# Kernel optimization log

Measured on AMD Instinct MI355X. Metric: run time of the kernel, lower is better.

The kernel has to match this reference:

```python
import jax, jax.numpy as jnp
import numpy as np
from jax import lax

SCORE_TH = 0.05
IOU_TH = 0.5
MAX_DET = 100  # fixed keep budget per class (torch version is variable-length; we pad)
BBOX_STD = jnp.array([0.1, 0.1, 0.2, 0.2], dtype=jnp.float32)


def setup_inputs() -> dict:
    key = jax.random.key(0)
    k1, k2, k3, k4 = jax.random.split(key, 4)
    A, C, H, W = 200000, 80, 768, 768
    # sigmoid-like scores, skewed low so the 0.05 threshold is meaningful
    classification = jax.random.uniform(k1, (A, C), dtype=jnp.float32) ** 4
    regression = jax.random.normal(k2, (A, 4), dtype=jnp.float32)
    ctr = jax.random.uniform(k3, (A, 2), dtype=jnp.float32, minval=0.0, maxval=float(W))
    wh = jax.random.uniform(k4, (A, 2), dtype=jnp.float32, minval=8.0, maxval=128.0)
    anchors = jnp.concatenate([ctr - 0.5 * wh, ctr + 0.5 * wh], axis=-1)  # valid x1y1x2y2
    return {"classification": classification, "regression": regression,
            "anchors": anchors, "img_h": H, "img_w": W}


def _decode_clip(anchors, regression, img_h, img_w):
    # BBoxTransform: RetinaNet delta decode with std [0.1,0.1,0.2,0.2], then ClipBoxes
    wa = anchors[:, 2] - anchors[:, 0]
    ha = anchors[:, 3] - anchors[:, 1]
    cxa = anchors[:, 0] + 0.5 * wa
    cya = anchors[:, 1] + 0.5 * ha
    d = regression * BBOX_STD
    cx = cxa + d[:, 0] * wa
    cy = cya + d[:, 1] * ha
    w = jnp.exp(d[:, 2]) * wa
    h = jnp.exp(d[:, 3]) * ha
    boxes = jnp.stack([cx - 0.5 * w, cy - 0.5 * h, cx + 0.5 * w, cy + 0.5 * h], axis=-1)
    lim = jnp.array([img_w, img_h, img_w, img_h], dtype=boxes.dtype)
    return jnp.clip(boxes, 0.0, lim)


def _nms_one(scores_c, boxes, areas):
    # greedy NMS for one class over all A anchors; fixed MAX_DET iterations
    s0 = jnp.where(scores_c > SCORE_TH, scores_c, -1.0)

    def step(s, _):
        i = jnp.argmax(s)
        valid = s[i] > 0.0
        b = boxes[i]
        xx1 = jnp.maximum(b[0], boxes[:, 0])
        yy1 = jnp.maximum(b[1], boxes[:, 1])
        xx2 = jnp.minimum(b[2], boxes[:, 2])
        yy2 = jnp.minimum(b[3], boxes[:, 3])
        inter = jnp.maximum(xx2 - xx1, 0.0) * jnp.maximum(yy2 - yy1, 0.0)
        iou = inter / (areas[i] + areas - inter)
        supp = (iou > IOU_TH) & valid
        s = jnp.where(supp, -1.0, s).at[i].set(-1.0)
        return s, (i, valid)

    _, (idx, val) = lax.scan(step, s0, None, length=MAX_DET)
    return idx, val  # [MAX_DET] int, [MAX_DET] bool


def _forward(classification, regression, anchors, img_h, img_w):
    boxes = _decode_clip(anchors, regression, img_h, img_w)  # [A,4]
    # NMS index selection is non-differentiable (as in torch); stop_gradient the selection path
    boxes_ng = lax.stop_gradient(boxes)
    scores_ng = lax.stop_gradient(classification)
    areas = (boxes_ng[:, 2] - boxes_ng[:, 0]) * (boxes_ng[:, 3] - boxes_ng[:, 1])
    idx, val = jax.vmap(_nms_one, in_axes=(1, None, None))(scores_ng, boxes_ng, areas)  # [C,M]
    C = classification.shape[1]
    sel_scores = jnp.take_along_axis(classification.T, idx, axis=1) * val          # [C,M]
    sel_boxes = boxes[idx] * val[..., None]                                        # [C,M,4]
    class_ids = jnp.where(val, jnp.arange(C, dtype=jnp.int32)[:, None], -1)        # [C,M]
    # torch returns variable-length concatenations; we return fixed-size padded
    # equivalents (invalid slots: score=0, class=-1, box=0)
    return sel_scores.reshape(-1), class_ids.reshape(-1), sel_boxes.reshape(-1, 4)


def reference(classification, regression, anchors, img_h, img_w):
    return _forward(classification, regression, anchors, img_h, img_w)
```

## Files before the change

kernel.cpp:

```cpp
#include <hip/hip_runtime.h>
#include <float.h>
#include <math.h>

#define SCORE_TH 0.05f
#define IOU_TH   0.5f
#define MAXD     100
#define CAP      512
#define HI_TH    0.996f
#define SWALK    192
#define NWORDS   3
#define CNT_STRIDE 16

__device__ __forceinline__ float4 decode_box(float4 an, float4 r, float W, float H)
{
    float wa = an.z - an.x, ha = an.w - an.y;
    float cxa = an.x + 0.5f * wa, cya = an.y + 0.5f * ha;
    float cx = cxa + r.x * 0.1f * wa;
    float cy = cya + r.y * 0.1f * ha;
    float w  = expf(r.z * 0.2f) * wa;
    float h  = expf(r.w * 0.2f) * ha;
    float x1 = cx - 0.5f * w, y1 = cy - 0.5f * h;
    float x2 = cx + 0.5f * w, y2 = cy + 0.5f * h;
    x1 = fminf(fmaxf(x1, 0.f), W);
    y1 = fminf(fmaxf(y1, 0.f), H);
    x2 = fminf(fmaxf(x2, 0.f), W);
    y2 = fminf(fmaxf(y2, 0.f), H);
    return make_float4(x1, y1, x2, y2);
}

template<int CC>
__global__ __launch_bounds__(256)
void k_compact(const float4* __restrict__ cls4, float2* __restrict__ cand,
               int* __restrict__ cnt, int* __restrict__ loflag,
               int C_rt, int total4)
{
    const int C = CC ? CC : C_rt;
    __shared__ unsigned char lflag[256];
    for (int i = threadIdx.x; i < C; i += blockDim.x) lflag[i] = 0;
    __syncthreads();

    const int gstride = gridDim.x * blockDim.x;
    const int gtid = blockIdx.x * blockDim.x + threadIdx.x;

    for (int j0 = gtid; j0 < total4; j0 += 4 * gstride) {
        int j1 = j0 + gstride, j2 = j0 + 2 * gstride, j3 = j0 + 3 * gstride;
        bool ok1 = j1 < total4, ok2 = j2 < total4, ok3 = j3 < total4;
        float4 v0 = cls4[j0];
        float4 v1 = ok1 ? cls4[j1] : make_float4(0.f, 0.f, 0.f, 0.f);
        float4 v2 = ok2 ? cls4[j2] : make_float4(0.f, 0.f, 0.f, 0.f);
        float4 v3 = ok3 ? cls4[j3] : make_float4(0.f, 0.f, 0.f, 0.f);

        #pragma unroll
        for (int w = 0; w < 4; w++) {
            float4 v = (w == 0) ? v0 : (w == 1) ? v1 : (w == 2) ? v2 : v3;
            if (w == 1 && !ok1) break;
            if (w == 2 && !ok2) break;
            if (w == 3 && !ok3) break;
            unsigned b = (unsigned)(j0 + w * gstride) * 4u;
            int c = (int)(b % (unsigned)C);
            int a = (int)(b / (unsigned)C);
            float s[4] = {v.x, v.y, v.z, v.w};
            #pragma unroll
            for (int j = 0; j < 4; j++) {
                float sc = s[j];
                if (sc > HI_TH) {
                    int pos = atomicAdd(&cnt[c * CNT_STRIDE], 1);
                    if (pos < CAP) cand[(size_t)c * CAP + pos] = make_float2(sc, __int_as_float(a));
                } else if (sc > SCORE_TH) {
                    lflag[c] = 1;
                }
                c++; if (c == C) { c = 0; a++; }
            }
        }
    }
    __syncthreads();
    for (int i = threadIdx.x; i < C; i += blockDim.x)
        if (lflag[i]) loflag[i] = 1;
}

__device__ void fallback_class(const float* __restrict__ cls,
                               const float4* __restrict__ anch, const float4* __restrict__ reg,
                               float W, float H, int A, int C, int c,
                               float* __restrict__ out)
{
    __shared__ float kx1[MAXD], ky1[MAXD], kx2[MAXD], ky2[MAXD], kar[MAXD];
    __shared__ float rs[4]; __shared__ int ra[4];
    __shared__ float cs; __shared__ int caid; __shared__ int have; __shared__ int suppflag;
    int lane = threadIdx.x & 63, wid = threadIdx.x >> 6;
    float s_last = FLT_MAX; int a_last = -1;
    int kept = 0;
    int total = C * MAXD;
    for (long long guard = 0; guard <= (long long)A && kept < MAXD; guard++) {
        float bs = -1.f; int ba = 0x7fffffff;
        for (int a = threadIdx.x; a < A; a += blockDim.x) {
            float s = cls[(size_t)a * C + c];
            if (s <= SCORE_TH) continue;
            if (s > s_last || (s == s_last && a <= a_last)) continue;
            if (s > bs || (s == bs && a < ba)) { bs = s; ba = a; }
        }
        for (int off = 32; off >= 1; off >>= 1) {
            float s2 = __shfl_down(bs, off);
            int a2 = __shfl_down(ba, off);
            if (s2 > bs || (s2 == bs && a2 < ba)) { bs = s2; ba = a2; }
        }
        if (lane == 0) { rs[wid] = bs; ra[wid] = ba; }
        __syncthreads();
        if (threadIdx.x == 0) {
            float fs = rs[0]; int fa = ra[0];
            for (int w = 1; w < 4; w++)
                if (rs[w] > fs || (rs[w] == fs && ra[w] < fa)) { fs = rs[w]; fa = ra[w]; }
            cs = fs; caid = fa; have = (fs > 0.f) ? 1 : 0;
        }
        __syncthreads();
        if (!have) break;
        float s_c = cs; int a_c = caid;
        s_last = s_c; a_last = a_c;
        float4 b = decode_box(anch[a_c], reg[a_c], W, H);
        float ar = (b.z - b.x) * (b.w - b.y);
        if (threadIdx.x == 0) suppflag = 0;
        __syncthreads();
        for (int k = threadIdx.x; k < kept; k += blockDim.x) {
            float xx1 = fmaxf(b.x, kx1[k]);
            float yy1 = fmaxf(b.y, ky1[k]);
            float xx2 = fminf(b.z, kx2[k]);
            float yy2 = fminf(b.w, ky2[k]);
            float inter = fmaxf(xx2 - xx1, 0.f) * fmaxf(yy2 - yy1, 0.f);
            float iou = inter / (ar + kar[k] - inter);
            if (iou > IOU_TH) suppflag = 1;
        }
        __syncthreads();
        if (!suppflag) {
            if (threadIdx.x == 0) {
                kx1[kept] = b.x; ky1[kept] = b.y; kx2[kept] = b.z; ky2[kept] = b.w; kar[kept] = ar;
                int slot = c * MAXD + kept;
                out[slot] = s_c;
                out[total + slot] = (float)c;
                float* ob = out + 2 * (size_t)total + (size_t)slot * 4;
                ob[0] = b.x; ob[1] = b.y; ob[2] = b.z; ob[3] = b.w;
            }
            kept++;
        }
        __syncthreads();
    }
    for (int k = kept + threadIdx.x; k < MAXD; k += blockDim.x) {
        int slot = c * MAXD + k;
        out[slot] = 0.f;
        out[total + slot] = -1.f;
        float* ob = out + 2 * (size_t)total + (size_t)slot * 4;
        ob[0] = 0.f; ob[1] = 0.f; ob[2] = 0.f; ob[3] = 0.f;
    }
}

__global__ __launch_bounds__(256)
void k_nms(const float* __restrict__ cls,
           const float4* __restrict__ anch, const float4* __restrict__ reg,
           const int* __restrict__ ph, const int* __restrict__ pw,
           const float2* __restrict__ cand, const int* __restrict__ cnt,
           const int* __restrict__ loflag,
           float* __restrict__ out, int A, int C)
{
    int c = blockIdx.x;
    __shared__ unsigned long long keys[CAP];
    __shared__ float bx1[SWALK], by1[SWALK], bx2[SWALK], by2[SWALK], sar[SWALK];
    __shared__ __align__(16) unsigned long long m0[SWALK], m1[SWALK], m2[SWALK];
    __shared__ int kidx[MAXD];

    float W = (float)(*pw), H = (float)(*ph);
    int n_raw = cnt[c * CNT_STRIDE];
    if (n_raw > CAP) {
        fallback_class(cls, anch, reg, W, H, A, C, c, out);
        return;
    }
    int n = n_raw;

    const int SORTN = (n <= 256) ? 256 : CAP;
    for (int i = threadIdx.x; i < SORTN; i += blockDim.x) {
        if (i < n) {
            float2 e = cand[(size_t)c * CAP + i];
            unsigned sbits = __float_as_uint(e.x);
            unsigned aid   = (unsigned)__float_as_int(e.y);
            keys[i] = ((unsigned long long)(~sbits) << 32) | (unsigned long long)aid;
        } else {
            keys[i] = 0xFFFFFFFFFFFFFFFFull;
        }
    }
    __syncthreads();

    for (int k = 2; k <= SORTN; k <<= 1) {
        for (int j = k >> 1; j > 0; j >>= 1) {
            for (int i = threadIdx.x; i < SORTN; i += blockDim.x) {
                int ixj = i ^ j;
                if (ixj > i) {
                    unsigned long long a = keys[i], b = keys[ixj];
                    bool sw = ((i & k) == 0) ? (a > b) : (a < b);
                    if (sw) { keys[i] = b; keys[ixj] = a; }
                }
            }
            __syncthreads();
        }
    }

    int nS = n < SWALK ? n : SWALK;
    for (int i = threadIdx.x; i < nS; i += blockDim.x) {
        unsigned aid = (unsigned)keys[i];
        float4 b = decode_box(anch[aid], reg[aid], W, H);
        bx1[i] = b.x; by1[i] = b.y; bx2[i] = b.z; by2[i] = b.w;
        sar[i] = (b.z - b.x) * (b.w - b.y);
    }
    __syncthreads();

    for (int task = threadIdx.x; task < nS * NWORDS; task += blockDim.x) {
        int i = task / NWORDS;
        int w = task - i * NWORDS;
        unsigned long long m = 0ull;
        int j0 = w << 6;
        int jend = j0 + 64 < nS ? j0 + 64 : nS;
        int js = j0 > i + 1 ? j0 : i + 1;
        float ix1 = bx1[i], iy1 = by1[i], ix2 = bx2[i], iy2 = by2[i], ia = sar[i];
        for (int j = js; j < jend; ++j) {
            float xx1 = fmaxf(ix1, bx1[j]);
            float yy1 = fmaxf(iy1, by1[j]);
            float xx2 = fminf(ix2, bx2[j]);
            float yy2 = fminf(iy2, by2[j]);
            float inter = fmaxf(xx2 - xx1, 0.f) * fmaxf(yy2 - yy1, 0.f);
            float iou = inter / (ia + sar[j] - inter);
            if (iou > IOU_TH) m |= 1ull << (j - j0);
        }
        if (w == 0) m0[i] = m; else if (w == 1) m1[i] = m; else m2[i] = m;
    }
    __syncthreads();

    unsigned long long rem0 = 0, rem1 = 0, rem2 = 0;
    int kept = 0;
    for (int k0 = 0; k0 < nS && kept < MAXD; k0 += 4) {
        ulonglong2 A0 = *(const ulonglong2*)&m0[k0];
        ulonglong2 A1 = *(const ulonglong2*)&m0[k0 + 2];
        ulonglong2 B0 = *(const ulonglong2*)&m1[k0];
        ulonglong2 B1 = *(const ulonglong2*)&m1[k0 + 2];
        ulonglong2 C0 = *(const ulonglong2*)&m2[k0];
        ulonglong2 C1 = *(const ulonglong2*)&m2[k0 + 2];
        unsigned long long g = A0.x | A0.y | A1.x | A1.y | B0.x | B0.y | B1.x | B1.y
                             | C0.x | C0.y | C1.x | C1.y;
        unsigned long long rw4 = ((k0 < 64) ? rem0 : (k0 < 128) ? rem1 : rem2) >> (k0 & 63);
        if (g == 0ull && (rw4 & 0xFull) == 0ull && k0 + 4 <= nS && kept + 4 <= MAXD) {
            if (threadIdx.x == 0) {
                kidx[kept] = k0; kidx[kept + 1] = k0 + 1;
                kidx[kept + 2] = k0 + 2; kidx[kept + 3] = k0 + 3;
            }
            kept += 4;
            continue;
        }
        #pragma unroll
        for (int s = 0; s < 4; ++s) {
            int k = k0 + s;
            if (k < nS && kept < MAXD) {
                unsigned long long mm0 = (s == 0) ? A0.x : (s == 1) ? A0.y : (s == 2) ? A1.x : A1.y;
                unsigned long long mm1 = (s == 0) ? B0.x : (s == 1) ? B0.y : (s == 2) ? B1.x : B1.y;
                unsigned long long mm2 = (s == 0) ? C0.x : (s == 1) ? C0.y : (s == 2) ? C1.x : C1.y;
                unsigned long long rw = (k < 64) ? rem0 : (k < 128) ? rem1 : rem2;
                if (!((rw >> (k & 63)) & 1ull)) {
                    if (threadIdx.x == 0) kidx[kept] = k;
                    ++kept;
                    rem0 |= mm0; rem1 |= mm1; rem2 |= mm2;
                }
            }
        }
    }
    __syncthreads();

    if (kept < MAXD && (n > nS || loflag[c] != 0)) {
        fallback_class(cls, anch, reg, W, H, A, C, c, out);
        return;
    }

    int total = C * MAXD;
    int base = c * MAXD;
    for (int m = threadIdx.x; m < kept; m += blockDim.x) {
        int k = kidx[m];
        unsigned long long key = keys[k];
        float sc = __uint_as_float(~(unsigned)(key >> 32));
        out[base + m] = sc;
        out[total + base + m] = (float)c;
        float* ob = out + 2 * (size_t)total + (size_t)(base + m) * 4;
        ob[0] = bx1[k]; ob[1] = by1[k]; ob[2] = bx2[k]; ob[3] = by2[k];
    }
    for (int m = kept + threadIdx.x; m < MAXD; m += blockDim.x) {
        out[base + m] = 0.f;
        out[total + base + m] = -1.f;
        float* ob = out + 2 * (size_t)total + (size_t)(base + m) * 4;
        ob[0] = 0.f; ob[1] = 0.f; ob[2] = 0.f; ob[3] = 0.f;
    }
}

extern "C" void kernel_launch(void* const* d_in, const int* in_sizes, int n_in,
                              void* d_out, int out_size, void* d_ws, size_t ws_size,
                              hipStream_t stream)
{
    const float*  cls  = (const float*)d_in[0];
    const float4* reg  = (const float4*)d_in[1];
    const float4* anch = (const float4*)d_in[2];
    const int*    ph   = (const int*)d_in[3];
    const int*    pw   = (const int*)d_in[4];
    int A = in_sizes[1] / 4;
    int C = in_sizes[0] / A;
    float* out = (float*)d_out;

    char* ws = (char*)d_ws;
    float2* cand = (float2*)ws;
    int* ctrl   = (int*)(cand + (size_t)C * CAP);
    int* cnt    = ctrl;
    int* loflag = ctrl + C * CNT_STRIDE;

    hipMemsetAsync(ctrl, 0, (C * CNT_STRIDE + C) * sizeof(int), stream);

    int total4 = (int)((long long)A * C / 4);
    int blocks2 = (total4 + 255) / 256;
    if (blocks2 > 2048) blocks2 = 2048;
    if (C == 80 && (long long)A * C < (1LL << 31))
        k_compact<80><<<blocks2, 256, 0, stream>>>((const float4*)cls, cand, cnt, loflag, C, total4);
    else
        k_compact<0><<<blocks2, 256, 0, stream>>>((const float4*)cls, cand, cnt, loflag, C, total4);

    k_nms<<<C, 256, 0, stream>>>(cls, anch, reg, ph, pw, cand, cnt, loflag, out, A, C);
}
```

Measured before the change: 140.3 us.

## Replace bitonic sort with rank-by-counting sort and prefetch mask words in walk

```diff
diff --git a/kernel.cpp b/kernel.cpp
--- a/kernel.cpp
+++ b/kernel.cpp
@@ -160,7 +160,8 @@
            float* __restrict__ out, int A, int C)
 {
     int c = blockIdx.x;
-    __shared__ unsigned long long keys[CAP];
+    __shared__ __align__(16) unsigned long long keys_raw[CAP];
+    __shared__ unsigned long long keys[SWALK];
     __shared__ float bx1[SWALK], by1[SWALK], bx2[SWALK], by2[SWALK], sar[SWALK];
     __shared__ __align__(16) unsigned long long m0[SWALK], m1[SWALK], m2[SWALK];
     __shared__ int kidx[MAXD];
@@ -172,40 +173,32 @@
         return;
     }
     int n = n_raw;
-
-    const int SORTN = (n <= 256) ? 256 : CAP;
-    for (int i = threadIdx.x; i < SORTN; i += blockDim.x) {
-        if (i < n) {
-            float2 e = cand[(size_t)c * CAP + i];
-            unsigned sbits = __float_as_uint(e.x);
-            unsigned aid   = (unsigned)__float_as_int(e.y);
-            keys[i] = ((unsigned long long)(~sbits) << 32) | (unsigned long long)aid;
-        } else {
-            keys[i] = 0xFFFFFFFFFFFFFFFFull;
-        }
-    }
-    __syncthreads();
-
-    for (int k = 2; k <= SORTN; k <<= 1) {
-        for (int j = k >> 1; j > 0; j >>= 1) {
-            for (int i = threadIdx.x; i < SORTN; i += blockDim.x) {
-                int ixj = i ^ j;
-                if (ixj > i) {
-                    unsigned long long a = keys[i], b = keys[ixj];
-                    bool sw = ((i & k) == 0) ? (a > b) : (a < b);
-                    if (sw) { keys[i] = b; keys[ixj] = a; }
-                }
-            }
-            __syncthreads();
-        }
-    }
-
     int nS = n < SWALK ? n : SWALK;
-    for (int i = threadIdx.x; i < nS; i += blockDim.x) {
-        unsigned aid = (unsigned)keys[i];
-        float4 b = decode_box(anch[aid], reg[aid], W, H);
-        bx1[i] = b.x; by1[i] = b.y; bx2[i] = b.z; by2[i] = b.w;
-        sar[i] = (b.z - b.x) * (b.w - b.y);
+
+    for (int i = threadIdx.x; i < n; i += blockDim.x) {
+        float2 e = cand[(size_t)c * CAP + i];
+        unsigned sbits = __float_as_uint(e.x);
+        unsigned aid   = (unsigned)__float_as_int(e.y);
+        keys_raw[i] = ((unsigned long long)(~sbits) << 32) | (unsigned long long)aid;
+    }
+    __syncthreads();
+
+    for (int i = threadIdx.x; i < n; i += blockDim.x) {
+        unsigned long long ki = keys_raw[i];
+        int r = 0;
+        int j = 0;
+        for (; j + 2 <= n; j += 2) {
+            ulonglong2 kj = *(const ulonglong2*)&keys_raw[j];
+            r += (kj.x < ki) + (kj.y < ki);
+        }
+        if (j < n) r += (keys_raw[j] < ki);
+        if (r < SWALK) {
+            keys[r] = ki;
+            unsigned aid = (unsigned)ki;
+            float4 b = decode_box(anch[aid], reg[aid], W, H);
+            bx1[r] = b.x; by1[r] = b.y; bx2[r] = b.z; by2[r] = b.w;
+            sar[r] = (b.z - b.x) * (b.w - b.y);
+        }
     }
     __syncthreads();
 
@@ -232,15 +225,19 @@
 
     unsigned long long rem0 = 0, rem1 = 0, rem2 = 0;
     int kept = 0;
+    ulonglong2 A0 = *(const ulonglong2*)&m0[0], A1 = *(const ulonglong2*)&m0[2];
+    ulonglong2 B0 = *(const ulonglong2*)&m1[0], B1 = *(const ulonglong2*)&m1[2];
+    ulonglong2 Q0 = *(const ulonglong2*)&m2[0], Q1 = *(const ulonglong2*)&m2[2];
     for (int k0 = 0; k0 < nS && kept < MAXD; k0 += 4) {
-        ulonglong2 A0 = *(const ulonglong2*)&m0[k0];
-        ulonglong2 A1 = *(const ulonglong2*)&m0[k0 + 2];
-        ulonglong2 B0 = *(const ulonglong2*)&m1[k0];
-        ulonglong2 B1 = *(const ulonglong2*)&m1[k0 + 2];
-        ulonglong2 C0 = *(const ulonglong2*)&m2[k0];
-        ulonglong2 C1 = *(const ulonglong2*)&m2[k0 + 2];
+        ulonglong2 nA0, nA1, nB0, nB1, nQ0, nQ1;
+        int kn = k0 + 4;
+        if (kn < nS) {
+            nA0 = *(const ulonglong2*)&m0[kn]; nA1 = *(const ulonglong2*)&m0[kn + 2];
+            nB0 = *(const ulonglong2*)&m1[kn]; nB1 = *(const ulonglong2*)&m1[kn + 2];
+            nQ0 = *(const ulonglong2*)&m2[kn]; nQ1 = *(const ulonglong2*)&m2[kn + 2];
+        }
         unsigned long long g = A0.x | A0.y | A1.x | A1.y | B0.x | B0.y | B1.x | B1.y
-                             | C0.x | C0.y | C1.x | C1.y;
+                             | Q0.x | Q0.y | Q1.x | Q1.y;
         unsigned long long rw4 = ((k0 < 64) ? rem0 : (k0 < 128) ? rem1 : rem2) >> (k0 & 63);
         if (g == 0ull && (rw4 & 0xFull) == 0ull && k0 + 4 <= nS && kept + 4 <= MAXD) {
             if (threadIdx.x == 0) {
@@ -248,23 +245,24 @@
                 kidx[kept + 2] = k0 + 2; kidx[kept + 3] = k0 + 3;
             }
             kept += 4;
-            continue;
-        }
-        #pragma unroll
-        for (int s = 0; s < 4; ++s) {
-            int k = k0 + s;
-            if (k < nS && kept < MAXD) {
-                unsigned long long mm0 = (s == 0) ? A0.x : (s == 1) ? A0.y : (s == 2) ? A1.x : A1.y;
-                unsigned long long mm1 = (s == 0) ? B0.x : (s == 1) ? B0.y : (s == 2) ? B1.x : B1.y;
-                unsigned long long mm2 = (s == 0) ? C0.x : (s == 1) ? C0.y : (s == 2) ? C1.x : C1.y;
-                unsigned long long rw = (k < 64) ? rem0 : (k < 128) ? rem1 : rem2;
-                if (!((rw >> (k & 63)) & 1ull)) {
-                    if (threadIdx.x == 0) kidx[kept] = k;
-                    ++kept;
-                    rem0 |= mm0; rem1 |= mm1; rem2 |= mm2;
+        } else {
+            #pragma unroll
+            for (int s = 0; s < 4; ++s) {
+                int k = k0 + s;
+                if (k < nS && kept < MAXD) {
+                    unsigned long long mm0 = (s == 0) ? A0.x : (s == 1) ? A0.y : (s == 2) ? A1.x : A1.y;
+                    unsigned long long mm1 = (s == 0) ? B0.x : (s == 1) ? B0.y : (s == 2) ? B1.x : B1.y;
+                    unsigned long long mm2 = (s == 0) ? Q0.x : (s == 1) ? Q0.y : (s == 2) ? Q1.x : Q1.y;
+                    unsigned long long rw = (k < 64) ? rem0 : (k < 128) ? rem1 : rem2;
+                    if (!((rw >> (k & 63)) & 1ull)) {
+                        if (threadIdx.x == 0) kidx[kept] = k;
+                        ++kept;
+                        rem0 |= mm0; rem1 |= mm1; rem2 |= mm2;
+                    }
                 }
             }
         }
+        A0 = nA0; A1 = nA1; B0 = nB0; B1 = nB1; Q0 = nQ0; Q1 = nQ1;
     }
     __syncthreads();
 
```

Measured after the change: 136.2 us. 3.0% less time.
